# Kernel optimization log

Measured on AMD Instinct MI355X. Metric: run time of the kernel, lower is better.

The kernel has to match this reference:

```python
import jax, jax.numpy as jnp
import numpy as np

N_NODES = 50000
N_EDGES = 800000
EMBED_DIM = 256
HIDDEN_DIM = 128
OUT_DIM = 12
N_TARGETS = 4096


def gcn_conv(x, edge_index, W, b):
    """PyG-style GCNConv: add self-loops, symmetric deg^-1/2 normalization,
    linear transform then sparse aggregation."""
    n = x.shape[0]
    loop = jnp.arange(n)
    src = jnp.concatenate([edge_index[0], loop])
    dst = jnp.concatenate([edge_index[1], loop])
    # degree of destination nodes (incl. self loops)
    deg = jax.ops.segment_sum(jnp.ones_like(dst, dtype=x.dtype), dst, num_segments=n)
    dinv = jnp.where(deg > 0, jax.lax.rsqrt(deg), 0.0)
    norm = dinv[src] * dinv[dst]                     # [E+n]
    h = x @ W                                        # [n, out] transform first (PyG order)
    msgs = h[src] * norm[:, None]                    # [E+n, out]
    return jax.ops.segment_sum(msgs, dst, num_segments=n) + b


def setup_inputs() -> dict:
    key = jax.random.key(0)
    ks = jax.random.split(key, 9)
    x = jax.random.normal(ks[0], (N_NODES, EMBED_DIM), dtype=jnp.float32)
    edge_index = jax.random.randint(ks[1], (2, N_EDGES), 0, N_NODES, dtype=jnp.int64)
    target_mask = jax.random.randint(ks[2], (N_TARGETS,), 0, N_NODES, dtype=jnp.int64)
    s1 = 1.0 / np.sqrt(EMBED_DIM)
    s2 = 1.0 / np.sqrt(HIDDEN_DIM)
    W1 = jax.random.uniform(ks[3], (EMBED_DIM, HIDDEN_DIM), jnp.float32, -s1, s1)
    b1 = jnp.zeros((HIDDEN_DIM,), jnp.float32)
    W2 = jax.random.uniform(ks[4], (HIDDEN_DIM, HIDDEN_DIM), jnp.float32, -s2, s2)
    b2 = jnp.zeros((HIDDEN_DIM,), jnp.float32)
    Wr = jax.random.uniform(ks[5], (HIDDEN_DIM, OUT_DIM), jnp.float32, -s2, s2)
    br = jax.random.uniform(ks[6], (OUT_DIM,), jnp.float32, -s2, s2)
    return {"x": x, "edge_index": edge_index, "target_mask": target_mask,
            "W1": W1, "b1": b1, "W2": W2, "b2": b2, "Wr": Wr, "br": br}


def reference(x, edge_index, target_mask, W1, b1, W2, b2, Wr, br):
    h = jax.nn.relu(gcn_conv(x, edge_index, W1, b1))
    h = jax.nn.relu(gcn_conv(h, edge_index, W2, b2))
    pred = h[target_mask] @ Wr + br                  # [N_TARGETS, OUT_DIM]
    return pred
```

## Files before the change

kernel.cpp:

```cpp
#include <hip/hip_runtime.h>
#include <math.h>

#define N_NODES 50000
#define N_EDGES 800000
#define EMBED 256
#define HID 128
#define OUTD 12
#define N_TGT 4096

#define SCAN_NB 196
#define NPART 8
#define NODES_PER_PART 6250
#define RCAP 64

typedef short bf16x8 __attribute__((ext_vector_type(8)));
typedef float f32x4 __attribute__((ext_vector_type(4)));
typedef int intx4 __attribute__((ext_vector_type(4)));

__device__ __forceinline__ unsigned short f2b(float f) {
    union { float f; unsigned int u; } v;
    v.f = f;
    unsigned int u = v.u;
    return (unsigned short)((u + 0x7FFFu + ((u >> 16) & 1u)) >> 16);
}

__device__ __forceinline__ float b2f(unsigned short s) {
    union { unsigned int u; float f; } v;
    v.u = ((unsigned int)s) << 16;
    return v.f;
}

__global__ __launch_bounds__(256) void k_prelude(int* __restrict__ counts,
                                                 const float* __restrict__ W1,
                                                 unsigned short* __restrict__ Wt1,
                                                 const float* __restrict__ W2,
                                                 unsigned short* __restrict__ Wt2) {
    int i = blockIdx.x * 256 + threadIdx.x;
    if (i < N_NODES) counts[i] = 0;
    if (i < 32768) {
        int nn = i >> 8, k = i & 255;
        Wt1[nn * 256 + k] = f2b(W1[(size_t)k * 128 + nn]);
    } else if (i < 49152) {
        int j = i - 32768;
        int nn = j >> 7, k = j & 127;
        Wt2[nn * 128 + k] = f2b(W2[(size_t)k * 128 + nn]);
    }
}

__global__ void k_fill_direct(const int* __restrict__ src, const int* __restrict__ dst,
                              int* __restrict__ counts, int* __restrict__ col_p, int nE4) {
    int g = blockIdx.x & (NPART - 1);
    int i = (blockIdx.x >> 3) * 256 + threadIdx.x;
    if (i >= nE4) return;
    intx4 d4 = *(const intx4*)&dst[i * 4];
    intx4 s4 = *(const intx4*)&src[i * 4];
#pragma unroll
    for (int q = 0; q < 4; ++q) {
        int d = d4[q];
        if ((unsigned)(d - g * NODES_PER_PART) < (unsigned)NODES_PER_PART) {
            int pos = atomicAdd(&counts[d], 1);
            if (pos < RCAP) col_p[d * RCAP + pos] = s4[q];
        }
    }
}

__global__ __launch_bounds__(256) void k_sort_dinv(const int* __restrict__ counts,
                                                   int* __restrict__ col_p,
                                                   float* __restrict__ dinv) {
    int wid = threadIdx.x >> 6;
    int lane = threadIdx.x & 63;
    int v = blockIdx.x * 4 + wid;
    if (v >= N_NODES) return;
    int cnt = counts[v];
    if (lane == 0) dinv[v] = rsqrtf(1.0f + (float)cnt);
    cnt = min(cnt, RCAP);
    if (cnt <= 1) return;
    int beg = v * RCAP;
    int key = (lane < cnt) ? col_p[beg + lane] : 0x7FFFFFFF;
#pragma unroll
    for (int k = 2; k <= 64; k <<= 1) {
#pragma unroll
        for (int j = k >> 1; j > 0; j >>= 1) {
            int other = __shfl_xor(key, j);
            bool up = ((lane & k) == 0);
            bool lower = ((lane & j) == 0);
            key = (lower == up) ? min(key, other) : max(key, other);
        }
    }
    if (lane < cnt) col_p[beg + lane] = key;
}

template <int K, bool IS_BF16>
__global__ __launch_bounds__(256) void k_gemm_mfma(const void* __restrict__ Xv,
                                                   const unsigned short* __restrict__ Wt,
                                                   unsigned short* __restrict__ Hb, int n) {
    __shared__ unsigned short As[64 * 40];
    const int tid = threadIdx.x;
    const int row0 = blockIdx.x * 64;
    const int w = tid >> 6, lane = tid & 63;
    const int lr = lane & 15, lg = lane >> 4;
    constexpr int NKS = K / 32;

    bf16x8 bfr[NKS][2];
#pragma unroll
    for (int ks = 0; ks < NKS; ++ks)
#pragma unroll
        for (int fn = 0; fn < 2; ++fn) {
            int colg = w * 32 + fn * 16 + lr;
            bfr[ks][fn] = *(const bf16x8*)&Wt[(size_t)colg * K + ks * 32 + lg * 8];
        }

    const int r0s = (tid * 2) >> 3, c0s = ((tid * 2) & 7) * 4;
    const int r1s = (tid * 2 + 1) >> 3, c1s = ((tid * 2 + 1) & 7) * 4;

    const float* Xf = (const float*)Xv;
    const unsigned short* Xb = (const unsigned short*)Xv;

    float4 f0 = make_float4(0.f, 0.f, 0.f, 0.f), f1 = f0;
    ushort4 u0 = make_ushort4(0, 0, 0, 0), u1 = u0;
    if (IS_BF16) {
        if (row0 + r0s < n) u0 = *(const ushort4*)&Xb[(size_t)(row0 + r0s) * K + c0s];
        if (row0 + r1s < n) u1 = *(const ushort4*)&Xb[(size_t)(row0 + r1s) * K + c1s];
    } else {
        if (row0 + r0s < n) f0 = *(const float4*)&Xf[(size_t)(row0 + r0s) * K + c0s];
        if (row0 + r1s < n) f1 = *(const float4*)&Xf[(size_t)(row0 + r1s) * K + c1s];
    }

    f32x4 acc[4][2] = {};
#pragma unroll
    for (int ks = 0; ks < NKS; ++ks) {
        __syncthreads();
        if (IS_BF16) {
            *(ushort4*)&As[r0s * 40 + c0s] = u0;
            *(ushort4*)&As[r1s * 40 + c1s] = u1;
        } else {
            *(ushort4*)&As[r0s * 40 + c0s] = make_ushort4(f2b(f0.x), f2b(f0.y), f2b(f0.z), f2b(f0.w));
            *(ushort4*)&As[r1s * 40 + c1s] = make_ushort4(f2b(f1.x), f2b(f1.y), f2b(f1.z), f2b(f1.w));
        }
        __syncthreads();
        if (ks + 1 < NKS) {
            int ko = (ks + 1) * 32;
            if (IS_BF16) {
                u0 = make_ushort4(0, 0, 0, 0); u1 = u0;
                if (row0 + r0s < n) u0 = *(const ushort4*)&Xb[(size_t)(row0 + r0s) * K + ko + c0s];
                if (row0 + r1s < n) u1 = *(const ushort4*)&Xb[(size_t)(row0 + r1s) * K + ko + c1s];
            } else {
                f0 = make_float4(0.f, 0.f, 0.f, 0.f); f1 = f0;
                if (row0 + r0s < n) f0 = *(const float4*)&Xf[(size_t)(row0 + r0s) * K + ko + c0s];
                if (row0 + r1s < n) f1 = *(const float4*)&Xf[(size_t)(row0 + r1s) * K + ko + c1s];
            }
        }
#pragma unroll
        for (int fm = 0; fm < 4; ++fm) {
            bf16x8 afr = *(const bf16x8*)&As[(fm * 16 + lr) * 40 + lg * 8];
#pragma unroll
            for (int fn = 0; fn < 2; ++fn)
                acc[fm][fn] = __builtin_amdgcn_mfma_f32_16x16x32_bf16(
                    afr, bfr[ks][fn], acc[fm][fn], 0, 0, 0);
        }
    }
#pragma unroll
    for (int fm = 0; fm < 4; ++fm) {
#pragma unroll
        for (int r = 0; r < 4; ++r) {
            int gr = row0 + fm * 16 + lg * 4 + r;
            if (gr < n) {
#pragma unroll
                for (int fn = 0; fn < 2; ++fn)
                    Hb[(size_t)gr * 128 + w * 32 + fn * 16 + lr] = f2b(acc[fm][fn][r]);
            }
        }
    }
}

__device__ __forceinline__ void agg_row(const unsigned short* __restrict__ h,
                                        const int* __restrict__ counts,
                                        const int* __restrict__ col_p,
                                        const float* __restrict__ dinv,
                                        const float* __restrict__ b,
                                        int v, int lane,
                                        unsigned short* __restrict__ dst16) {
    float dv = dinv[v];
    ushort4 hv = *(const ushort4*)&h[(size_t)v * HID + lane * 4];
    float sl = dv * dv;
    f32x4 a0 = {b2f(hv.x) * sl, b2f(hv.y) * sl, b2f(hv.z) * sl, b2f(hv.w) * sl};
    f32x4 a1 = {0.f, 0.f, 0.f, 0.f}, a2 = a1, a3 = a1;
    int beg = v * RCAP;
    int cnt = min(counts[v], RCAP);
    for (int j0 = 0; j0 < cnt; j0 += 32) {
        int m = cnt - j0; if (m > 32) m = 32;
        int sj = 0; float wj = 0.f;
        if (lane < m) {
            sj = col_p[beg + j0 + lane];
            wj = dinv[sj] * dv;
        }
        int M = (m + 3) & ~3;
        float w0 = __shfl(wj, 0, 32), w1 = __shfl(wj, 1, 32);
        float w2 = __shfl(wj, 2, 32), w3 = __shfl(wj, 3, 32);
        int s0 = __shfl(sj, 0, 32), s1 = __shfl(sj, 1, 32);
        int s2 = __shfl(sj, 2, 32), s3 = __shfl(sj, 3, 32);
        ushort4 q0 = *(const ushort4*)&h[(size_t)s0 * HID + lane * 4];
        ushort4 q1 = *(const ushort4*)&h[(size_t)s1 * HID + lane * 4];
        ushort4 q2 = *(const ushort4*)&h[(size_t)s2 * HID + lane * 4];
        ushort4 q3 = *(const ushort4*)&h[(size_t)s3 * HID + lane * 4];
        for (int jj = 0; jj < M; jj += 4) {
            ushort4 n0 = q0, n1 = q1, n2 = q2, n3 = q3;
            float nw0 = 0.f, nw1 = 0.f, nw2 = 0.f, nw3 = 0.f;
            if (jj + 4 < M) {
                int t0 = __shfl(sj, jj + 4, 32), t1 = __shfl(sj, jj + 5, 32);
                int t2 = __shfl(sj, jj + 6, 32), t3 = __shfl(sj, jj + 7, 32);
                nw0 = __shfl(wj, jj + 4, 32); nw1 = __shfl(wj, jj + 5, 32);
                nw2 = __shfl(wj, jj + 6, 32); nw3 = __shfl(wj, jj + 7, 32);
                n0 = *(const ushort4*)&h[(size_t)t0 * HID + lane * 4];
                n1 = *(const ushort4*)&h[(size_t)t1 * HID + lane * 4];
                n2 = *(const ushort4*)&h[(size_t)t2 * HID + lane * 4];
                n3 = *(const ushort4*)&h[(size_t)t3 * HID + lane * 4];
            }
            a0[0] = fmaf(b2f(q0.x), w0, a0[0]); a0[1] = fmaf(b2f(q0.y), w0, a0[1]);
            a0[2] = fmaf(b2f(q0.z), w0, a0[2]); a0[3] = fmaf(b2f(q0.w), w0, a0[3]);
            a1[0] = fmaf(b2f(q1.x), w1, a1[0]); a1[1] = fmaf(b2f(q1.y), w1, a1[1]);
            a1[2] = fmaf(b2f(q1.z), w1, a1[2]); a1[3] = fmaf(b2f(q1.w), w1, a1[3]);
            a2[0] = fmaf(b2f(q2.x), w2, a2[0]); a2[1] = fmaf(b2f(q2.y), w2, a2[1]);
            a2[2] = fmaf(b2f(q2.z), w2, a2[2]); a2[3] = fmaf(b2f(q2.w), w2, a2[3]);
            a3[0] = fmaf(b2f(q3.x), w3, a3[0]); a3[1] = fmaf(b2f(q3.y), w3, a3[1]);
            a3[2] = fmaf(b2f(q3.z), w3, a3[2]); a3[3] = fmaf(b2f(q3.w), w3, a3[3]);
            q0 = n0; q1 = n1; q2 = n2; q3 = n3;
            w0 = nw0; w1 = nw1; w2 = nw2; w3 = nw3;
        }
    }
    float4 bv = *(const float4*)&b[lane * 4];
    ushort4 r;
    r.x = f2b(fmaxf((a0[0] + a1[0]) + (a2[0] + a3[0]) + bv.x, 0.f));
    r.y = f2b(fmaxf((a0[1] + a1[1]) + (a2[1] + a3[1]) + bv.y, 0.f));
    r.z = f2b(fmaxf((a0[2] + a1[2]) + (a2[2] + a3[2]) + bv.z, 0.f));
    r.w = f2b(fmaxf((a0[3] + a1[3]) + (a2[3] + a3[3]) + bv.w, 0.f));
    *(ushort4*)dst16 = r;
}

__global__ __launch_bounds__(256) void k_agg_all(const unsigned short* __restrict__ h,
                                                 const int* __restrict__ counts,
                                                 const int* __restrict__ col_p,
                                                 const float* __restrict__ dinv,
                                                 const float* __restrict__ b,
                                                 unsigned short* __restrict__ out) {
    int t = blockIdx.x * 256 + threadIdx.x;
    int v = t >> 5;
    int lane = t & 31;
    if (v >= N_NODES) return;
    agg_row(h, counts, col_p, dinv, b, v, lane, &out[(size_t)v * HID + lane * 4]);
}

__global__ __launch_bounds__(256) void k_agg_tgt(const unsigned short* __restrict__ h,
                                                 const int* __restrict__ counts,
                                                 const int* __restrict__ col_p,
                                                 const float* __restrict__ dinv,
                                                 const int* __restrict__ tgt,
                                                 const float* __restrict__ b,
                                                 unsigned short* __restrict__ out2) {
    int t = blockIdx.x * 256 + threadIdx.x;
    int tt = t >> 5;
    int lane = t & 31;
    if (tt >= N_TGT) return;
    int v = tgt[tt];
    agg_row(h, counts, col_p, dinv, b, v, lane, &out2[(size_t)tt * HID + lane * 4]);
}

__global__ void k_final(const unsigned short* __restrict__ h2t,
                        const float* __restrict__ Wr, const float* __restrict__ br,
                        float* __restrict__ out) {
    int t = blockIdx.x;
    int lane = threadIdx.x;
    ushort2 hv = *(const ushort2*)&h2t[(size_t)t * HID + lane * 2];
    float h0 = b2f(hv.x), h1 = b2f(hv.y);
#pragma unroll
    for (int j = 0; j < OUTD; ++j) {
        float p = h0 * Wr[(lane * 2) * OUTD + j] + h1 * Wr[(lane * 2 + 1) * OUTD + j];
#pragma unroll
        for (int off = 32; off > 0; off >>= 1) p += __shfl_down(p, off);
        if (lane == 0) out[t * OUTD + j] = p + br[j];
    }
}

extern "C" void kernel_launch(void* const* d_in, const int* in_sizes, int n_in,
                              void* d_out, int out_size, void* d_ws, size_t ws_size,
                              hipStream_t stream) {
    const float* x  = (const float*)d_in[0];
    const int*   ei = (const int*)d_in[1];
    const int*   tm = (const int*)d_in[2];
    const float* W1 = (const float*)d_in[3];
    const float* b1 = (const float*)d_in[4];
    const float* W2 = (const float*)d_in[5];
    const float* b2 = (const float*)d_in[6];
    const float* Wr = (const float*)d_in[7];
    const float* br = (const float*)d_in[8];
    float* out = (float*)d_out;

    const int* e_src = ei;
    const int* e_dst = ei + N_EDGES;

    char* ws = (char*)d_ws;
    float*          dinv   = (float*)(ws + 0x000000);
    int*            counts = (int*)  (ws + 0x040000);
    unsigned short* Wt1    = (unsigned short*)(ws + 0x080000);
    unsigned short* Wt2    = (unsigned short*)(ws + 0x090000);
    unsigned short* out2   = (unsigned short*)(ws + 0x0A0000);
    int*            col_p  = (int*)  (ws + 0x200000);
    unsigned short* bufA   = (unsigned short*)(ws + 0xE40000);
    unsigned short* bufB   = (unsigned short*)(ws + 0x1B00000);

    const int NE4     = N_EDGES / 4;
    const int NB_EP   = ((NE4 + 255) / 256) * NPART;
    const int NB_AGG  = (N_NODES * 32 + 255) / 256;
    const int NB_AGT  = (N_TGT * 32 + 255) / 256;
    const int NB_MF   = (N_NODES + 63) / 64;
    const int NB_SORT = (N_NODES + 3) / 4;

    k_prelude<<<SCAN_NB, 256, 0, stream>>>(counts, W1, Wt1, W2, Wt2);
    k_fill_direct<<<NB_EP, 256, 0, stream>>>(e_src, e_dst, counts, col_p, NE4);
    k_sort_dinv<<<NB_SORT, 256, 0, stream>>>(counts, col_p, dinv);

    k_gemm_mfma<EMBED, false><<<NB_MF, 256, 0, stream>>>(x, Wt1, bufA, N_NODES);
    k_agg_all<<<NB_AGG, 256, 0, stream>>>(bufA, counts, col_p, dinv, b1, bufB);

    k_gemm_mfma<HID, true><<<NB_MF, 256, 0, stream>>>(bufB, Wt2, bufA, N_NODES);
    k_agg_tgt<<<NB_AGT, 256, 0, stream>>>(bufA, counts, col_p, dinv, tm, b2, out2);

    k_final<<<N_TGT, 64, 0, stream>>>(out2, Wr, br, out);
}
```

Before: 147.8 us.

## Co-schedule layer-1 GEMM with edge fill and fuse target aggregation with readout

The first GEMM and the CSR edge-fill now run in one launch, with block ranges split between the two independent jobs so the compute-bound GEMM overlaps the atomic-heavy scatter. The target aggregation kernel is merged with the final linear readout, so the intermediate bf16 target buffer and one launch are gone. The readout now uses a 32-lane shuffle reduction over the values already in registers. The risk is that the fused kernel's mixed block types contend for CUs, and that it keeps GEMM-sized register and LDS use for the fill blocks.

```diff
diff --git a/kernel.cpp b/kernel.cpp
--- a/kernel.cpp
+++ b/kernel.cpp
@@ -12,6 +12,7 @@
 #define NPART 8
 #define NODES_PER_PART 6250
 #define RCAP 64
+#define NB_G1 782
 
 typedef short bf16x8 __attribute__((ext_vector_type(8)));
 typedef float f32x4 __attribute__((ext_vector_type(4)));
@@ -47,10 +48,103 @@
     }
 }
 
-__global__ void k_fill_direct(const int* __restrict__ src, const int* __restrict__ dst,
-                              int* __restrict__ counts, int* __restrict__ col_p, int nE4) {
-    int g = blockIdx.x & (NPART - 1);
-    int i = (blockIdx.x >> 3) * 256 + threadIdx.x;
+template <int K, bool IS_BF16>
+__device__ __forceinline__ void gemm_body(int gb, int tid, const void* __restrict__ Xv,
+                                          const unsigned short* __restrict__ Wt,
+                                          unsigned short* __restrict__ Hb, int n,
+                                          unsigned short* As ) {
+    const int row0 = gb * 64;
+    const int w = tid >> 6, lane = tid & 63;
+    const int lr = lane & 15, lg = lane >> 4;
+    constexpr int NKS = K / 32;
+
+    bf16x8 bfr[NKS][2];
+#pragma unroll
+    for (int ks = 0; ks < NKS; ++ks)
+#pragma unroll
+        for (int fn = 0; fn < 2; ++fn) {
+            int colg = w * 32 + fn * 16 + lr;
+            bfr[ks][fn] = *(const bf16x8*)&Wt[(size_t)colg * K + ks * 32 + lg * 8];
+        }
+
+    const int r0s = (tid * 2) >> 3, c0s = ((tid * 2) & 7) * 4;
+    const int r1s = (tid * 2 + 1) >> 3, c1s = ((tid * 2 + 1) & 7) * 4;
+
+    const float* Xf = (const float*)Xv;
+    const unsigned short* Xb = (const unsigned short*)Xv;
+
+    float4 f0 = make_float4(0.f, 0.f, 0.f, 0.f), f1 = f0;
+    ushort4 u0 = make_ushort4(0, 0, 0, 0), u1 = u0;
+    if (IS_BF16) {
+        if (row0 + r0s < n) u0 = *(const ushort4*)&Xb[(size_t)(row0 + r0s) * K + c0s];
+        if (row0 + r1s < n) u1 = *(const ushort4*)&Xb[(size_t)(row0 + r1s) * K + c1s];
+    } else {
+        if (row0 + r0s < n) f0 = *(const float4*)&Xf[(size_t)(row0 + r0s) * K + c0s];
+        if (row0 + r1s < n) f1 = *(const float4*)&Xf[(size_t)(row0 + r1s) * K + c1s];
+    }
+
+    f32x4 acc[4][2] = {};
+#pragma unroll
+    for (int ks = 0; ks < NKS; ++ks) {
+        __syncthreads();
+        if (IS_BF16) {
+            *(ushort4*)&As[r0s * 40 + c0s] = u0;
+            *(ushort4*)&As[r1s * 40 + c1s] = u1;
+        } else {
+            *(ushort4*)&As[r0s * 40 + c0s] = make_ushort4(f2b(f0.x), f2b(f0.y), f2b(f0.z), f2b(f0.w));
+            *(ushort4*)&As[r1s * 40 + c1s] = make_ushort4(f2b(f1.x), f2b(f1.y), f2b(f1.z), f2b(f1.w));
+        }
+        __syncthreads();
+        if (ks + 1 < NKS) {
+            int ko = (ks + 1) * 32;
+            if (IS_BF16) {
+                u0 = make_ushort4(0, 0, 0, 0); u1 = u0;
+                if (row0 + r0s < n) u0 = *(const ushort4*)&Xb[(size_t)(row0 + r0s) * K + ko + c0s];
+                if (row0 + r1s < n) u1 = *(const ushort4*)&Xb[(size_t)(row0 + r1s) * K + ko + c1s];
+            } else {
+                f0 = make_float4(0.f, 0.f, 0.f, 0.f); f1 = f0;
+                if (row0 + r0s < n) f0 = *(const float4*)&Xf[(size_t)(row0 + r0s) * K + ko + c0s];
+                if (row0 + r1s < n) f1 = *(const float4*)&Xf[(size_t)(row0 + r1s) * K + ko + c1s];
+            }
+        }
+#pragma unroll
+        for (int fm = 0; fm < 4; ++fm) {
+            bf16x8 afr = *(const bf16x8*)&As[(fm * 16 + lr) * 40 + lg * 8];
+#pragma unroll
+            for (int fn = 0; fn < 2; ++fn)
+                acc[fm][fn] = __builtin_amdgcn_mfma_f32_16x16x32_bf16(
+                    afr, bfr[ks][fn], acc[fm][fn], 0, 0, 0);
+        }
+    }
+#pragma unroll
+    for (int fm = 0; fm < 4; ++fm) {
+#pragma unroll
+        for (int r = 0; r < 4; ++r) {
+            int gr = row0 + fm * 16 + lg * 4 + r;
+            if (gr < n) {
+#pragma unroll
+                for (int fn = 0; fn < 2; ++fn)
+                    Hb[(size_t)gr * 128 + w * 32 + fn * 16 + lr] = f2b(acc[fm][fn][r]);
+            }
+        }
+    }
+}
+
+__global__ __launch_bounds__(256) void k_fused1(const float* __restrict__ x,
+                                                const unsigned short* __restrict__ Wt1,
+                                                unsigned short* __restrict__ bufA,
+                                                const int* __restrict__ src,
+                                                const int* __restrict__ dst,
+                                                int* __restrict__ counts,
+                                                int* __restrict__ col_p, int nE4) {
+    __shared__ unsigned short As[64 * 40];
+    const int b = blockIdx.x, tid = threadIdx.x;
+    if (b < NB_G1) {
+        gemm_body<EMBED, false>(b, tid, x, Wt1, bufA, N_NODES, As);
+        return;
+    }
+    int g = b & (NPART - 1);
+    int i = ((b - NB_G1) >> 3) * 256 + tid;
     if (i >= nE4) return;
     intx4 d4 = *(const intx4*)&dst[i * 4];
     intx4 s4 = *(const intx4*)&src[i * 4];
@@ -62,6 +156,13 @@
             if (pos < RCAP) col_p[d * RCAP + pos] = s4[q];
         }
     }
+}
+
+__global__ __launch_bounds__(256) void k_gemm2(const unsigned short* __restrict__ X,
+                                               const unsigned short* __restrict__ Wt,
+                                               unsigned short* __restrict__ Hb, int n) {
+    __shared__ unsigned short As[64 * 40];
+    gemm_body<HID, true>(blockIdx.x, threadIdx.x, X, Wt, Hb, n, As);
 }
 
 __global__ __launch_bounds__(256) void k_sort_dinv(const int* __restrict__ counts,
@@ -90,96 +191,11 @@
     if (lane < cnt) col_p[beg + lane] = key;
 }
 
-template <int K, bool IS_BF16>
-__global__ __launch_bounds__(256) void k_gemm_mfma(const void* __restrict__ Xv,
-                                                   const unsigned short* __restrict__ Wt,
-                                                   unsigned short* __restrict__ Hb, int n) {
-    __shared__ unsigned short As[64 * 40];
-    const int tid = threadIdx.x;
-    const int row0 = blockIdx.x * 64;
-    const int w = tid >> 6, lane = tid & 63;
-    const int lr = lane & 15, lg = lane >> 4;
-    constexpr int NKS = K / 32;
-
-    bf16x8 bfr[NKS][2];
-#pragma unroll
-    for (int ks = 0; ks < NKS; ++ks)
-#pragma unroll
-        for (int fn = 0; fn < 2; ++fn) {
-            int colg = w * 32 + fn * 16 + lr;
-            bfr[ks][fn] = *(const bf16x8*)&Wt[(size_t)colg * K + ks * 32 + lg * 8];
-        }
-
-    const int r0s = (tid * 2) >> 3, c0s = ((tid * 2) & 7) * 4;
-    const int r1s = (tid * 2 + 1) >> 3, c1s = ((tid * 2 + 1) & 7) * 4;
-
-    const float* Xf = (const float*)Xv;
-    const unsigned short* Xb = (const unsigned short*)Xv;
-
-    float4 f0 = make_float4(0.f, 0.f, 0.f, 0.f), f1 = f0;
-    ushort4 u0 = make_ushort4(0, 0, 0, 0), u1 = u0;
-    if (IS_BF16) {
-        if (row0 + r0s < n) u0 = *(const ushort4*)&Xb[(size_t)(row0 + r0s) * K + c0s];
-        if (row0 + r1s < n) u1 = *(const ushort4*)&Xb[(size_t)(row0 + r1s) * K + c1s];
-    } else {
-        if (row0 + r0s < n) f0 = *(const float4*)&Xf[(size_t)(row0 + r0s) * K + c0s];
-        if (row0 + r1s < n) f1 = *(const float4*)&Xf[(size_t)(row0 + r1s) * K + c1s];
-    }
-
-    f32x4 acc[4][2] = {};
-#pragma unroll
-    for (int ks = 0; ks < NKS; ++ks) {
-        __syncthreads();
-        if (IS_BF16) {
-            *(ushort4*)&As[r0s * 40 + c0s] = u0;
-            *(ushort4*)&As[r1s * 40 + c1s] = u1;
-        } else {
-            *(ushort4*)&As[r0s * 40 + c0s] = make_ushort4(f2b(f0.x), f2b(f0.y), f2b(f0.z), f2b(f0.w));
-            *(ushort4*)&As[r1s * 40 + c1s] = make_ushort4(f2b(f1.x), f2b(f1.y), f2b(f1.z), f2b(f1.w));
-        }
-        __syncthreads();
-        if (ks + 1 < NKS) {
-            int ko = (ks + 1) * 32;
-            if (IS_BF16) {
-                u0 = make_ushort4(0, 0, 0, 0); u1 = u0;
-                if (row0 + r0s < n) u0 = *(const ushort4*)&Xb[(size_t)(row0 + r0s) * K + ko + c0s];
-                if (row0 + r1s < n) u1 = *(const ushort4*)&Xb[(size_t)(row0 + r1s) * K + ko + c1s];
-            } else {
-                f0 = make_float4(0.f, 0.f, 0.f, 0.f); f1 = f0;
-                if (row0 + r0s < n) f0 = *(const float4*)&Xf[(size_t)(row0 + r0s) * K + ko + c0s];
-                if (row0 + r1s < n) f1 = *(const float4*)&Xf[(size_t)(row0 + r1s) * K + ko + c1s];
-            }
-        }
-#pragma unroll
-        for (int fm = 0; fm < 4; ++fm) {
-            bf16x8 afr = *(const bf16x8*)&As[(fm * 16 + lr) * 40 + lg * 8];
-#pragma unroll
-            for (int fn = 0; fn < 2; ++fn)
-                acc[fm][fn] = __builtin_amdgcn_mfma_f32_16x16x32_bf16(
-                    afr, bfr[ks][fn], acc[fm][fn], 0, 0, 0);
-        }
-    }
-#pragma unroll
-    for (int fm = 0; fm < 4; ++fm) {
-#pragma unroll
-        for (int r = 0; r < 4; ++r) {
-            int gr = row0 + fm * 16 + lg * 4 + r;
-            if (gr < n) {
-#pragma unroll
-                for (int fn = 0; fn < 2; ++fn)
-                    Hb[(size_t)gr * 128 + w * 32 + fn * 16 + lr] = f2b(acc[fm][fn][r]);
-            }
-        }
-    }
-}
-
-__device__ __forceinline__ void agg_row(const unsigned short* __restrict__ h,
-                                        const int* __restrict__ counts,
-                                        const int* __restrict__ col_p,
-                                        const float* __restrict__ dinv,
-                                        const float* __restrict__ b,
-                                        int v, int lane,
-                                        unsigned short* __restrict__ dst16) {
+__device__ __forceinline__ f32x4 agg_core(const unsigned short* __restrict__ h,
+                                          const int* __restrict__ counts,
+                                          const int* __restrict__ col_p,
+                                          const float* __restrict__ dinv,
+                                          int v, int lane) {
     float dv = dinv[v];
     ushort4 hv = *(const ushort4*)&h[(size_t)v * HID + lane * 4];
     float sl = dv * dv;
@@ -228,13 +244,12 @@
             w0 = nw0; w1 = nw1; w2 = nw2; w3 = nw3;
         }
     }
-    float4 bv = *(const float4*)&b[lane * 4];
-    ushort4 r;
-    r.x = f2b(fmaxf((a0[0] + a1[0]) + (a2[0] + a3[0]) + bv.x, 0.f));
-    r.y = f2b(fmaxf((a0[1] + a1[1]) + (a2[1] + a3[1]) + bv.y, 0.f));
-    r.z = f2b(fmaxf((a0[2] + a1[2]) + (a2[2] + a3[2]) + bv.z, 0.f));
-    r.w = f2b(fmaxf((a0[3] + a1[3]) + (a2[3] + a3[3]) + bv.w, 0.f));
-    *(ushort4*)dst16 = r;
+    f32x4 r;
+    r[0] = (a0[0] + a1[0]) + (a2[0] + a3[0]);
+    r[1] = (a0[1] + a1[1]) + (a2[1] + a3[1]);
+    r[2] = (a0[2] + a1[2]) + (a2[2] + a3[2]);
+    r[3] = (a0[3] + a1[3]) + (a2[3] + a3[3]);
+    return r;
 }
 
 __global__ __launch_bounds__(256) void k_agg_all(const unsigned short* __restrict__ h,
@@ -247,37 +262,44 @@
     int v = t >> 5;
     int lane = t & 31;
     if (v >= N_NODES) return;
-    agg_row(h, counts, col_p, dinv, b, v, lane, &out[(size_t)v * HID + lane * 4]);
-}
-
-__global__ __launch_bounds__(256) void k_agg_tgt(const unsigned short* __restrict__ h,
-                                                 const int* __restrict__ counts,
-                                                 const int* __restrict__ col_p,
-                                                 const float* __restrict__ dinv,
-                                                 const int* __restrict__ tgt,
-                                                 const float* __restrict__ b,
-                                                 unsigned short* __restrict__ out2) {
+    f32x4 a = agg_core(h, counts, col_p, dinv, v, lane);
+    float4 bv = *(const float4*)&b[lane * 4];
+    ushort4 r;
+    r.x = f2b(fmaxf(a[0] + bv.x, 0.f));
+    r.y = f2b(fmaxf(a[1] + bv.y, 0.f));
+    r.z = f2b(fmaxf(a[2] + bv.z, 0.f));
+    r.w = f2b(fmaxf(a[3] + bv.w, 0.f));
+    *(ushort4*)&out[(size_t)v * HID + lane * 4] = r;
+}
+
+__global__ __launch_bounds__(256) void k_agg_tgt_final(const unsigned short* __restrict__ h,
+                                                       const int* __restrict__ counts,
+                                                       const int* __restrict__ col_p,
+                                                       const float* __restrict__ dinv,
+                                                       const int* __restrict__ tgt,
+                                                       const float* __restrict__ b,
+                                                       const float* __restrict__ Wr,
+                                                       const float* __restrict__ br,
+                                                       float* __restrict__ out) {
     int t = blockIdx.x * 256 + threadIdx.x;
     int tt = t >> 5;
     int lane = t & 31;
     if (tt >= N_TGT) return;
     int v = tgt[tt];
-    agg_row(h, counts, col_p, dinv, b, v, lane, &out2[(size_t)tt * HID + lane * 4]);
-}
-
-__global__ void k_final(const unsigned short* __restrict__ h2t,
-                        const float* __restrict__ Wr, const float* __restrict__ br,
-                        float* __restrict__ out) {
-    int t = blockIdx.x;
-    int lane = threadIdx.x;
-    ushort2 hv = *(const ushort2*)&h2t[(size_t)t * HID + lane * 2];
-    float h0 = b2f(hv.x), h1 = b2f(hv.y);
+    f32x4 a = agg_core(h, counts, col_p, dinv, v, lane);
+    float4 bv = *(const float4*)&b[lane * 4];
+    float r0 = fmaxf(a[0] + bv.x, 0.f);
+    float r1 = fmaxf(a[1] + bv.y, 0.f);
+    float r2 = fmaxf(a[2] + bv.z, 0.f);
+    float r3 = fmaxf(a[3] + bv.w, 0.f);
+    const float* wr = &Wr[lane * 4 * OUTD];
 #pragma unroll
     for (int j = 0; j < OUTD; ++j) {
-        float p = h0 * Wr[(lane * 2) * OUTD + j] + h1 * Wr[(lane * 2 + 1) * OUTD + j];
-#pragma unroll
-        for (int off = 32; off > 0; off >>= 1) p += __shfl_down(p, off);
-        if (lane == 0) out[t * OUTD + j] = p + br[j];
+        float p = r0 * wr[0 * OUTD + j] + r1 * wr[1 * OUTD + j] +
+                  r2 * wr[2 * OUTD + j] + r3 * wr[3 * OUTD + j];
+#pragma unroll
+        for (int off = 16; off > 0; off >>= 1) p += __shfl_down(p, off, 32);
+        if (lane == 0) out[tt * OUTD + j] = p + br[j];
     }
 }
 
@@ -303,27 +325,23 @@
     int*            counts = (int*)  (ws + 0x040000);
     unsigned short* Wt1    = (unsigned short*)(ws + 0x080000);
     unsigned short* Wt2    = (unsigned short*)(ws + 0x090000);
-    unsigned short* out2   = (unsigned short*)(ws + 0x0A0000);
     int*            col_p  = (int*)  (ws + 0x200000);
     unsigned short* bufA   = (unsigned short*)(ws + 0xE40000);
     unsigned short* bufB   = (unsigned short*)(ws + 0x1B00000);
 
     const int NE4     = N_EDGES / 4;
-    const int NB_EP   = ((NE4 + 255) / 256) * NPART;
+    const int NB_FILL = ((NE4 + 255) / 256) * NPART;
+    const int NB_F1   = NB_G1 + NB_FILL;
     const int NB_AGG  = (N_NODES * 32 + 255) / 256;
     const int NB_AGT  = (N_TGT * 32 + 255) / 256;
-    const int NB_MF   = (N_NODES + 63) / 64;
     const int NB_SORT = (N_NODES + 3) / 4;
 
     k_prelude<<<SCAN_NB, 256, 0, stream>>>(counts, W1, Wt1, W2, Wt2);
-    k_fill_direct<<<NB_EP, 256, 0, stream>>>(e_src, e_dst, counts, col_p, NE4);
+    k_fused1<<<NB_F1, 256, 0, stream>>>(x, Wt1, bufA, e_src, e_dst, counts, col_p, NE4);
     k_sort_dinv<<<NB_SORT, 256, 0, stream>>>(counts, col_p, dinv);
 
-    k_gemm_mfma<EMBED, false><<<NB_MF, 256, 0, stream>>>(x, Wt1, bufA, N_NODES);
     k_agg_all<<<NB_AGG, 256, 0, stream>>>(bufA, counts, col_p, dinv, b1, bufB);
 
-    k_gemm_mfma<HID, true><<<NB_MF, 256, 0, stream>>>(bufB, Wt2, bufA, N_NODES);
-    k_agg_tgt<<<NB_AGT, 256, 0, stream>>>(bufA, counts, col_p, dinv, tm, b2, out2);
-
-    k_final<<<N_TGT, 64, 0, stream>>>(out2, Wr, br, out);
-}
+    k_gemm2<<<NB_G1, 256, 0, stream>>>(bufB, Wt2, bufA, N_NODES);
+    k_agg_tgt_final<<<NB_AGT, 256, 0, stream>>>(bufA, counts, col_p, dinv, tm, b2, Wr, br, out);
+}
```

New measurement: 135.8 us. 8.1% less time.
